# Performance work log

Hardware: AMD Instinct MI355X
Metric: run time of the kernel (lower is better)

Reference implementation:

```python
import jax, jax.numpy as jnp
import numpy as np

N = 50000      # nodes
E = 600000     # edges
D_IN = 128
D_H = 128
D_OUT = 64
HEADS = 2
NEG_SLOPE = 0.2  # PyG GATConv default leaky_relu slope
BN_EPS = 1e-5


def setup_inputs() -> dict:
    key = jax.random.key(0)
    ks = jax.random.split(key, 24)
    w = lambda i, shape: (jax.random.normal(ks[i], shape, jnp.float32) * 0.1)
    return {
        "x": jax.random.normal(ks[0], (N, D_IN), jnp.float32),
        "edge_index": jax.random.randint(ks[1], (2, E), 0, N, jnp.int64),
        "W_gcn1": w(2, (D_IN, D_H)),
        "b_gcn1": jnp.zeros((D_H,), jnp.float32),
        "bn1_gamma": jax.random.uniform(ks[3], (D_H,), jnp.float32, 0.5, 1.5),
        "bn1_beta": w(4, (D_H,)),
        "bn1_mean": w(5, (D_H,)),
        "bn1_var": jax.random.uniform(ks[6], (D_H,), jnp.float32, 0.5, 1.5),
        "W_gat1": w(7, (D_H, HEADS * D_H)),
        "a_src1": w(8, (HEADS, D_H)),
        "a_dst1": w(9, (HEADS, D_H)),
        "b_gat1": jnp.zeros((D_H,), jnp.float32),
        "W_gcn2": w(10, (D_H, D_H)),
        "b_gcn2": jnp.zeros((D_H,), jnp.float32),
        "bn2_gamma": jax.random.uniform(ks[11], (D_H,), jnp.float32, 0.5, 1.5),
        "bn2_beta": w(12, (D_H,)),
        "bn2_mean": w(13, (D_H,)),
        "bn2_var": jax.random.uniform(ks[14], (D_H,), jnp.float32, 0.5, 1.5),
        "W_gat2": w(15, (D_H, HEADS * D_OUT)),
        "a_src2": w(16, (HEADS, D_OUT)),
        "a_dst2": w(17, (HEADS, D_OUT)),
        "b_gat2": jnp.zeros((D_OUT,), jnp.float32),
    }


def _add_self_loops(edge_index):
    loop = jnp.arange(N, dtype=edge_index.dtype)
    src = jnp.concatenate([edge_index[0], loop])
    dst = jnp.concatenate([edge_index[1], loop])
    return src, dst


def _gcn(x, edge_index, W, b):
    # PyG GCNConv: add self-loops, symmetric D^-1/2 (A+I) D^-1/2 normalization
    src, dst = _add_self_loops(edge_index)
    deg = jax.ops.segment_sum(jnp.ones_like(dst, x.dtype), dst, num_segments=N)
    dinv = jax.lax.rsqrt(jnp.maximum(deg, 1.0))  # deg >= 1 with self-loops
    norm = dinv[src] * dinv[dst]                 # [E+N]
    h = x @ W                                    # [N, C]
    out = jax.ops.segment_sum(h[src] * norm[:, None], dst, num_segments=N)
    return out + b


def _gat(x, edge_index, W, a_src, a_dst, b, out_ch):
    # PyG GATConv (concat=False): per-head attention, segment softmax over dst,
    # mean across heads. Dropout off (eval mode).
    h = (x @ W).reshape(N, HEADS, out_ch)                 # [N, H, C]
    al_s = jnp.einsum('nhc,hc->nh', h, a_src)             # [N, H]
    al_d = jnp.einsum('nhc,hc->nh', h, a_dst)             # [N, H]
    src, dst = _add_self_loops(edge_index)
    e = al_s[src] + al_d[dst]                             # [E+N, H]
    e = jnp.where(e > 0, e, NEG_SLOPE * e)                # leaky_relu
    m = jax.ops.segment_max(e, dst, num_segments=N)       # [N, H]
    ex = jnp.exp(e - m[dst])
    denom = jax.ops.segment_sum(ex, dst, num_segments=N)  # [N, H]
    alpha = ex / denom[dst]                               # [E+N, H]
    out = jax.ops.segment_sum(h[src] * alpha[:, :, None], dst, num_segments=N)
    return out.mean(axis=1) + b                           # concat=False -> mean


def _bn_eval(x, gamma, beta, mean, var):
    return (x - mean) * jax.lax.rsqrt(var + BN_EPS) * gamma + beta


def reference(x, edge_index, W_gcn1, b_gcn1, bn1_gamma, bn1_beta, bn1_mean, bn1_var,
              W_gat1, a_src1, a_dst1, b_gat1, W_gcn2, b_gcn2,
              bn2_gamma, bn2_beta, bn2_mean, bn2_var,
              W_gat2, a_src2, a_dst2, b_gat2):
    h = _gcn(x, edge_index, W_gcn1, b_gcn1)
    h = jax.nn.relu(_bn_eval(h, bn1_gamma, bn1_beta, bn1_mean, bn1_var))
    h = jax.nn.relu(_gat(h, edge_index, W_gat1, a_src1, a_dst1, b_gat1, D_H))
    h = _gcn(h, edge_index, W_gcn2, b_gcn2)
    h = jax.nn.relu(_bn_eval(h, bn2_gamma, bn2_beta, bn2_mean, bn2_var))
    h = _gat(h, edge_index, W_gat2, a_src2, a_dst2, b_gat2, D_OUT)
    return jax.nn.log_softmax(h, axis=1)
```

## Files before the change

kernel.cpp:

```cpp
#include <hip/hip_runtime.h>
#include <hip/hip_bf16.h>

#define N_NODES 50000
#define N_EDGES 600000

typedef short bf16x8 __attribute__((ext_vector_type(8)));
typedef float f32x4 __attribute__((ext_vector_type(4)));

__device__ __forceinline__ float leaky(float e) { return fmaxf(e, 0.2f * e); }
__device__ __forceinline__ unsigned short f2b(float f) {
  __hip_bfloat16 h = __float2bfloat16(f);
  return *reinterpret_cast<unsigned short*>(&h);
}
__device__ __forceinline__ float blo(unsigned int u) { return __uint_as_float(u << 16); }
__device__ __forceinline__ float bhi(unsigned int u) { return __uint_as_float(u & 0xffff0000u); }

__global__ void k_convert(const int* __restrict__ e, int* __restrict__ src32,
                          int* __restrict__ dst32, int* __restrict__ deg,
                          const float* __restrict__ W1, const float* __restrict__ WG1,
                          const float* __restrict__ W2, const float* __restrict__ WG2,
                          unsigned short* __restrict__ Wt1, unsigned short* __restrict__ WtG1,
                          unsigned short* __restrict__ Wt2, unsigned short* __restrict__ WtG2,
                          const float* b1, const float* g1, const float* be1, const float* m1,
                          const float* v1, const float* b2, const float* g2, const float* be2,
                          const float* m2, const float* v2, float* sc1, float* sh1,
                          float* sc2, float* sh2,
                          const float* as1, const float* ad1, const float* as2,
                          const float* ad2, float* was1, float* wad1, float* was2,
                          float* wad2) {
  __shared__ int sflag;
  int tid = threadIdx.x;
  if (tid < 64) {
    int idx = 1 + 2 * tid * 4096;
    int v = e[idx];
    unsigned long long nz = __ballot(v != 0);
    if (tid == 0) sflag = (nz == 0ULL) ? 1 : 0;
  }
  __syncthreads();
  int f = sflag;
  int i = blockIdx.x * 256 + tid;
  if (i < N_EDGES) {
    int s, d;
    if (f) { s = e[2 * i]; d = e[2 * (N_EDGES + i)]; }
    else   { s = e[i];     d = e[N_EDGES + i]; }
    src32[i] = s;
    dst32[i] = d;
    atomicAdd(&deg[d], 1);
  }
  if (i < 16384) {
    int k = i >> 7, c = i & 127;
    Wt1[c * 128 + k] = f2b(W1[i]);
  } else if (i < 49152) {
    int l = i - 16384;
    int k = l >> 8, c = l & 255;
    WtG1[c * 128 + k] = f2b(WG1[l]);
  } else if (i < 65536) {
    int l = i - 49152;
    int k = l >> 7, c = l & 127;
    Wt2[c * 128 + k] = f2b(W2[l]);
  } else if (i < 81920) {
    int l = i - 65536;
    int k = l >> 7, c = l & 127;
    WtG2[c * 128 + k] = f2b(WG2[l]);
  } else if (i < 82048) {
    int c = i - 81920;
    float s = g1[c] * rsqrtf(v1[c] + 1e-5f);
    sc1[c] = s;
    sh1[c] = (b1[c] - m1[c]) * s + be1[c];
  } else if (i < 82176) {
    int c = i - 82048;
    float s = g2[c] * rsqrtf(v2[c] + 1e-5f);
    sc2[c] = s;
    sh2[c] = (b2[c] - m2[c]) * s + be2[c];
  } else if (i < 82688) {
    int j = i - 82176;
    int k = j & 127;
    int vec = j >> 7;
    const float* Wr = (vec < 2) ? (WG1 + k * 256) : (WG2 + k * 128);
    const float* av = (vec == 0) ? as1 : (vec == 1) ? ad1 : (vec == 2) ? as2 : ad2;
    float* op = (vec == 0) ? was1 : (vec == 1) ? wad1 : (vec == 2) ? was2 : wad2;
    int hl = (vec < 2) ? 128 : 64;
    float s0 = 0.f, s1 = 0.f;
    for (int c = 0; c < hl; c += 4) {
      float4 wv = *(const float4*)(Wr + c);
      float4 a4 = *(const float4*)(av + c);
      s0 += wv.x * a4.x + wv.y * a4.y + wv.z * a4.z + wv.w * a4.w;
    }
    for (int c = 0; c < hl; c += 4) {
      float4 wv = *(const float4*)(Wr + hl + c);
      float4 a4 = *(const float4*)(av + hl + c);
      s1 += wv.x * a4.x + wv.y * a4.y + wv.z * a4.z + wv.w * a4.w;
    }
    op[2 * k] = s0;
    op[2 * k + 1] = s1;
  }
}

__global__ void k_offsets(const int* __restrict__ deg, int* __restrict__ gbase,
                          int* __restrict__ roff, int* __restrict__ cursor,
                          float* __restrict__ dinv) {
  __shared__ int s[256];
  __shared__ int base;
  int t = threadIdx.x;
  int i = blockIdx.x * 256 + t;
  int v = (i < N_NODES) ? deg[i] : 0;
  s[t] = v;
  __syncthreads();
  for (int o = 1; o < 256; o <<= 1) {
    int x = (t >= o) ? s[t - o] : 0;
    __syncthreads();
    s[t] += x;
    __syncthreads();
  }
  if (t == 255) base = atomicAdd(gbase, s[255]);
  __syncthreads();
  int off = base + s[t] - v;
  if (i < N_NODES) {
    roff[i] = off;
    cursor[i] = off;
    dinv[i] = rsqrtf((float)v + 1.f);
  }
}
__global__ void k_fill(const int* __restrict__ src, const int* __restrict__ dst,
                       int* __restrict__ cursor, int2* __restrict__ aen,
                       const float* __restrict__ dinv) {
  int e = blockIdx.x * 256 + threadIdx.x;
  if (e < N_EDGES) {
    int s = src[e], d = dst[e];
    int pos = atomicAdd(&cursor[d], 1);
    aen[pos] = make_int2(s, __float_as_int(dinv[s]));
  }
}

__device__ __forceinline__ float4 ld4(const float* X, size_t idx) {
  return *(const float4*)(X + idx);
}
__device__ __forceinline__ float4 ld4(const unsigned short* X, size_t idx) {
  uint2 r = *(const uint2*)(X + idx);
  return make_float4(blo(r.x), bhi(r.x), blo(r.y), bhi(r.y));
}

template <int C, typename TX>
__global__ __launch_bounds__(256, 4) void gemm_mfma(const TX* __restrict__ X,
                                                    const unsigned short* __restrict__ Wt,
                                                    unsigned short* __restrict__ Hb) {
  constexpr int CTW = C / 64;
  __shared__ __align__(16) short smem[64 * 136];
  int tid = threadIdx.x;
  int row0 = blockIdx.x * 64;
  for (int i = tid; i < 2048; i += 256) {
    int r = i >> 5;
    int k4 = (i & 31) * 4;
    int row = row0 + r;
    float4 v = make_float4(0.f, 0.f, 0.f, 0.f);
    if (row < N_NODES) v = ld4(X, (size_t)row * 128 + k4);
    uint2 p;
    p.x = (unsigned int)f2b(v.x) | ((unsigned int)f2b(v.y) << 16);
    p.y = (unsigned int)f2b(v.z) | ((unsigned int)f2b(v.w) << 16);
    *(uint2*)&smem[r * 136 + k4] = p;
  }
  int wave = tid >> 6, lane = tid & 63;
  int m = lane & 15, quad = lane >> 4;
  int c0 = wave * (16 * CTW);
  bf16x8 b[CTW][4];
#pragma unroll
  for (int ct = 0; ct < CTW; ++ct) {
    const unsigned short* wp = Wt + (size_t)(c0 + ct * 16 + m) * 128 + quad * 8;
#pragma unroll
    for (int kk = 0; kk < 4; ++kk) b[ct][kk] = *(const bf16x8*)(wp + kk * 32);
  }
  __syncthreads();
#pragma unroll
  for (int rt = 0; rt < 4; ++rt) {
    bf16x8 a[4];
#pragma unroll
    for (int kk = 0; kk < 4; ++kk)
      a[kk] = *(const bf16x8*)&smem[(rt * 16 + m) * 136 + kk * 32 + quad * 8];
    f32x4 acc[CTW];
#pragma unroll
    for (int ct = 0; ct < CTW; ++ct) acc[ct] = (f32x4){0.f, 0.f, 0.f, 0.f};
#pragma unroll
    for (int ct = 0; ct < CTW; ++ct)
#pragma unroll
      for (int kk = 0; kk < 4; ++kk)
        acc[ct] = __builtin_amdgcn_mfma_f32_16x16x32_bf16(a[kk], b[ct][kk], acc[ct], 0, 0, 0);
    int rbase = row0 + rt * 16 + quad * 4;
#pragma unroll
    for (int ct = 0; ct < CTW; ++ct) {
#pragma unroll
      for (int reg = 0; reg < 4; ++reg) {
        int row = rbase + reg;
        if (row < N_NODES)
          Hb[(size_t)row * C + c0 + ct * 16 + m] = f2b(acc[ct][reg]);
      }
    }
  }
}

__global__ __launch_bounds__(256) void gcn_pull(const unsigned short* __restrict__ Hb,
                                                const int2* __restrict__ aen,
                                                const int* __restrict__ roff,
                                                const int* __restrict__ deg,
                                                const float* __restrict__ dinv,
                                                const float* __restrict__ sc,
                                                const float* __restrict__ sh,
                                                const float* __restrict__ was,
                                                const float* __restrict__ wad,
                                                float* __restrict__ als,
                                                float* __restrict__ ald,
                                                unsigned short* __restrict__ out) {
  int wv = (blockIdx.x * 256 + threadIdx.x) >> 6;
  int lane = threadIdx.x & 63;
  int q4 = lane >> 4, l16 = lane & 15;
  int qb = lane & 48, l7 = lane & 7;
  int i = 4 * wv + q4;
  if (i >= N_NODES) return;
  int off = roff[i], end = off + deg[i];
  float di = dinv[i];
  uint4 u = *(const uint4*)((const char*)Hb + (unsigned)i * 256u + l16 * 16u);
  float a0 = blo(u.x) * di, a1 = bhi(u.x) * di;
  float a2 = blo(u.y) * di, a3 = bhi(u.y) * di;
  float a4 = blo(u.z) * di, a5 = bhi(u.z) * di;
  float a6 = blo(u.w) * di, a7 = bhi(u.w) * di;
  int j = off;
  int nfull = (end - off) >> 3;
  int2 ae = make_int2(i, 0);
  if (l7 < end - j) ae = aen[j + l7];
  for (int t = 0; t < nfull; ++t) {
    int ss[8];
#pragma unroll
    for (int k = 0; k < 8; ++k) ss[k] = __shfl(ae.x, qb + k, 64);
    float ww[8];
#pragma unroll
    for (int k = 0; k < 8; ++k) ww[k] = __shfl(__int_as_float(ae.y), qb + k, 64);
    uint4 vv[8];
#pragma unroll
    for (int k = 0; k < 8; ++k)
      vv[k] = *(const uint4*)((const char*)Hb + (unsigned)ss[k] * 256u + l16 * 16u);
    j += 8;
    if (l7 < end - j) ae = aen[j + l7];
#pragma unroll
    for (int k = 0; k < 8; ++k) {
      a0 = fmaf(blo(vv[k].x), ww[k], a0); a1 = fmaf(bhi(vv[k].x), ww[k], a1);
      a2 = fmaf(blo(vv[k].y), ww[k], a2); a3 = fmaf(bhi(vv[k].y), ww[k], a3);
      a4 = fmaf(blo(vv[k].z), ww[k], a4); a5 = fmaf(bhi(vv[k].z), ww[k], a5);
      a6 = fmaf(blo(vv[k].w), ww[k], a6); a7 = fmaf(bhi(vv[k].w), ww[k], a7);
    }
  }
  int rem = end - j;
  if (rem) {
    int ss[8];
#pragma unroll
    for (int k = 0; k < 8; ++k) ss[k] = __shfl(ae.x, qb + k, 64);
    float ww[8];
#pragma unroll
    for (int k = 0; k < 8; ++k) ww[k] = __shfl(__int_as_float(ae.y), qb + k, 64);
    uint4 vv[8];
#pragma unroll
    for (int k = 0; k < 8; ++k)
      if (k < rem)
        vv[k] = *(const uint4*)((const char*)Hb + (unsigned)ss[k] * 256u + l16 * 16u);
#pragma unroll
    for (int k = 0; k < 8; ++k)
      if (k < rem) {
        a0 = fmaf(blo(vv[k].x), ww[k], a0); a1 = fmaf(bhi(vv[k].x), ww[k], a1);
        a2 = fmaf(blo(vv[k].y), ww[k], a2); a3 = fmaf(bhi(vv[k].y), ww[k], a3);
        a4 = fmaf(blo(vv[k].z), ww[k], a4); a5 = fmaf(bhi(vv[k].z), ww[k], a5);
        a6 = fmaf(blo(vv[k].w), ww[k], a6); a7 = fmaf(bhi(vv[k].w), ww[k], a7);
      }
  }
  int c0 = l16 * 8;
  float4 sca = *(const float4*)(sc + c0), scb = *(const float4*)(sc + c0 + 4);
  float4 sha = *(const float4*)(sh + c0), shb = *(const float4*)(sh + c0 + 4);
  float t0 = fmaxf(fmaf(a0 * di, sca.x, sha.x), 0.f);
  float t1 = fmaxf(fmaf(a1 * di, sca.y, sha.y), 0.f);
  float t2 = fmaxf(fmaf(a2 * di, sca.z, sha.z), 0.f);
  float t3 = fmaxf(fmaf(a3 * di, sca.w, sha.w), 0.f);
  float t4 = fmaxf(fmaf(a4 * di, scb.x, shb.x), 0.f);
  float t5 = fmaxf(fmaf(a5 * di, scb.y, shb.y), 0.f);
  float t6 = fmaxf(fmaf(a6 * di, scb.z, shb.z), 0.f);
  float t7 = fmaxf(fmaf(a7 * di, scb.w, shb.w), 0.f);
  float4 w0 = *(const float4*)(was + 2 * c0);
  float4 w1 = *(const float4*)(was + 2 * c0 + 4);
  float4 w2 = *(const float4*)(was + 2 * c0 + 8);
  float4 w3 = *(const float4*)(was + 2 * c0 + 12);
  float sl0 = t0 * w0.x + t1 * w0.z + t2 * w1.x + t3 * w1.z +
              t4 * w2.x + t5 * w2.z + t6 * w3.x + t7 * w3.z;
  float sl1 = t0 * w0.y + t1 * w0.w + t2 * w1.y + t3 * w1.w +
              t4 * w2.y + t5 * w2.w + t6 * w3.y + t7 * w3.w;
  w0 = *(const float4*)(wad + 2 * c0);
  w1 = *(const float4*)(wad + 2 * c0 + 4);
  w2 = *(const float4*)(wad + 2 * c0 + 8);
  w3 = *(const float4*)(wad + 2 * c0 + 12);
  float dl0 = t0 * w0.x + t1 * w0.z + t2 * w1.x + t3 * w1.z +
              t4 * w2.x + t5 * w2.z + t6 * w3.x + t7 * w3.z;
  float dl1 = t0 * w0.y + t1 * w0.w + t2 * w1.y + t3 * w1.w +
              t4 * w2.y + t5 * w2.w + t6 * w3.y + t7 * w3.w;
#pragma unroll
  for (int mask = 1; mask <= 8; mask <<= 1) {
    sl0 += __shfl_xor(sl0, mask, 64);
    sl1 += __shfl_xor(sl1, mask, 64);
    dl0 += __shfl_xor(dl0, mask, 64);
    dl1 += __shfl_xor(dl1, mask, 64);
  }
  if (l16 == 0) {
    *(float2*)(als + 2 * i) = make_float2(sl0, sl1);
    *(float2*)(ald + 2 * i) = make_float2(dl0, dl1);
  }
  uint4 pw;
  pw.x = (unsigned int)f2b(t0) | ((unsigned int)f2b(t1) << 16);
  pw.y = (unsigned int)f2b(t2) | ((unsigned int)f2b(t3) << 16);
  pw.z = (unsigned int)f2b(t4) | ((unsigned int)f2b(t5) << 16);
  pw.w = (unsigned int)f2b(t6) | ((unsigned int)f2b(t7) << 16);
  *(uint4*)(out + (size_t)i * 128 + l16 * 8) = pw;
}

__global__ __launch_bounds__(256) void gat_pull128(const unsigned short* __restrict__ Hb,
                                                   const int2* __restrict__ aen,
                                                   const int* __restrict__ roff,
                                                   const int* __restrict__ deg,
                                                   const float* __restrict__ als,
                                                   const float* __restrict__ ald,
                                                   const float* __restrict__ bias,
                                                   unsigned short* __restrict__ out) {
  int wv = (blockIdx.x * 256 + threadIdx.x) >> 6;
  int lane = threadIdx.x & 63;
  int half = lane >> 5, l = lane & 31;
  int hbase = lane & 32, l7 = lane & 7;
  int i = 2 * wv + half;
  if (i >= N_NODES) return;
  int off = roff[i], end = off + deg[i];
  int head = l >> 4;
  float2 dif = *(const float2*)(ald + 2 * i);
  float p = 0.f;
  float acc0 = 0.f, acc1 = 0.f, acc2 = 0.f, acc3 = 0.f;
  float acc4 = 0.f, acc5 = 0.f, acc6 = 0.f, acc7 = 0.f;
  int j = off;
  int nfull = (end - off) >> 3;
  int2 ae = make_int2(i, 0);
  float2 av = make_float2(-1e30f, -1e30f);
  if (l7 < end - j) {
    ae = aen[j + l7];
    av = *(const float2*)(als + 2 * ae.x);
  }
  for (int t = 0; t < nfull; ++t) {
    int ss[8];
#pragma unroll
    for (int k = 0; k < 8; ++k) ss[k] = __shfl(ae.x, hbase + k, 64);
    uint4 vv[8];
#pragma unroll
    for (int k = 0; k < 8; ++k)
      vv[k] = *(const uint4*)((const char*)Hb + (unsigned)ss[k] * 512u + l * 16u);
    float q0 = __expf(leaky(av.x + dif.x));
    float q1 = __expf(leaky(av.y + dif.y));
    j += 8;
    if (l7 < end - j) {
      ae = aen[j + l7];
      av = *(const float2*)(als + 2 * ae.x);
    }
#pragma unroll
    for (int k = 0; k < 8; ++k) {
      float b0 = __shfl(q0, hbase + k, 64);
      float b1 = __shfl(q1, hbase + k, 64);
      float q = head ? b1 : b0;
      p += q;
      acc0 = fmaf(q, blo(vv[k].x), acc0); acc1 = fmaf(q, bhi(vv[k].x), acc1);
      acc2 = fmaf(q, blo(vv[k].y), acc2); acc3 = fmaf(q, bhi(vv[k].y), acc3);
      acc4 = fmaf(q, blo(vv[k].z), acc4); acc5 = fmaf(q, bhi(vv[k].z), acc5);
      acc6 = fmaf(q, blo(vv[k].w), acc6); acc7 = fmaf(q, bhi(vv[k].w), acc7);
    }
  }
  int rem = end - j;
  if (rem) {
    int ss[8];
#pragma unroll
    for (int k = 0; k < 8; ++k) ss[k] = __shfl(ae.x, hbase + k, 64);
    uint4 vv[8];
#pragma unroll
    for (int k = 0; k < 8; ++k)
      if (k < rem)
        vv[k] = *(const uint4*)((const char*)Hb + (unsigned)ss[k] * 512u + l * 16u);
    float q0 = __expf(leaky(av.x + dif.x));
    float q1 = __expf(leaky(av.y + dif.y));
#pragma unroll
    for (int k = 0; k < 8; ++k)
      if (k < rem) {
        float b0 = __shfl(q0, hbase + k, 64);
        float b1 = __shfl(q1, hbase + k, 64);
        float q = head ? b1 : b0;
        p += q;
        acc0 = fmaf(q, blo(vv[k].x), acc0); acc1 = fmaf(q, bhi(vv[k].x), acc1);
        acc2 = fmaf(q, blo(vv[k].y), acc2); acc3 = fmaf(q, bhi(vv[k].y), acc3);
        acc4 = fmaf(q, blo(vv[k].z), acc4); acc5 = fmaf(q, bhi(vv[k].z), acc5);
        acc6 = fmaf(q, blo(vv[k].w), acc6); acc7 = fmaf(q, bhi(vv[k].w), acc7);
      }
  }
  float2 ai = *(const float2*)(als + 2 * i);
  float axs = head ? ai.y : ai.x;
  float dh = head ? dif.y : dif.x;
  float es = __expf(leaky(axs + dh));
  float rsel = 0.5f / (p + es);
  uint4 u = *(const uint4*)((const char*)Hb + (unsigned)i * 512u + l * 16u);
  acc0 = (acc0 + es * blo(u.x)) * rsel; acc1 = (acc1 + es * bhi(u.x)) * rsel;
  acc2 = (acc2 + es * blo(u.y)) * rsel; acc3 = (acc3 + es * bhi(u.y)) * rsel;
  acc4 = (acc4 + es * blo(u.z)) * rsel; acc5 = (acc5 + es * bhi(u.z)) * rsel;
  acc6 = (acc6 + es * blo(u.w)) * rsel; acc7 = (acc7 + es * bhi(u.w)) * rsel;
  acc0 += __shfl_xor(acc0, 16, 64); acc1 += __shfl_xor(acc1, 16, 64);
  acc2 += __shfl_xor(acc2, 16, 64); acc3 += __shfl_xor(acc3, 16, 64);
  acc4 += __shfl_xor(acc4, 16, 64); acc5 += __shfl_xor(acc5, 16, 64);
  acc6 += __shfl_xor(acc6, 16, 64); acc7 += __shfl_xor(acc7, 16, 64);
  if (head == 0) {
    int c = l * 8;
    float4 b0 = *(const float4*)(bias + c);
    float4 b1 = *(const float4*)(bias + c + 4);
    uint4 pw;
    pw.x = (unsigned int)f2b(fmaxf(acc0 + b0.x, 0.f)) |
           ((unsigned int)f2b(fmaxf(acc1 + b0.y, 0.f)) << 16);
    pw.y = (unsigned int)f2b(fmaxf(acc2 + b0.z, 0.f)) |
           ((unsigned int)f2b(fmaxf(acc3 + b0.w, 0.f)) << 16);
    pw.z = (unsigned int)f2b(fmaxf(acc4 + b1.x, 0.f)) |
           ((unsigned int)f2b(fmaxf(acc5 + b1.y, 0.f)) << 16);
    pw.w = (unsigned int)f2b(fmaxf(acc6 + b1.z, 0.f)) |
           ((unsigned int)f2b(fmaxf(acc7 + b1.w, 0.f)) << 16);
    *(uint4*)(out + (size_t)i * 128 + c) = pw;
  }
}

__global__ __launch_bounds__(256) void gat_pull64_lsm(const unsigned short* __restrict__ Hb,
                                                      const int2* __restrict__ aen,
                                                      const int* __restrict__ roff,
                                                      const int* __restrict__ deg,
                                                      const float* __restrict__ als,
                                                      const float* __restrict__ ald,
                                                      const float* __restrict__ bias,
                                                      float* __restrict__ out) {
  int wv = (blockIdx.x * 256 + threadIdx.x) >> 6;
  int lane = threadIdx.x & 63;
  int q4 = lane >> 4, l16 = lane & 15;
  int qb = lane & 48, l7 = lane & 7;
  int hh = l16 >> 3, p8 = l16 & 7;
  int i = 4 * wv + q4;
  if (i >= N_NODES) return;
  int off = roff[i], end = off + deg[i];
  unsigned cb2 = (unsigned)(hh * 64 + 8 * p8) * 2u;
  float2 dd = *(const float2*)(ald + 2 * i);
  float p = 0.f;
  float acc0 = 0.f, acc1 = 0.f, acc2 = 0.f, acc3 = 0.f;
  float acc4 = 0.f, acc5 = 0.f, acc6 = 0.f, acc7 = 0.f;
  int j = off;
  int nfull = (end - off) >> 3;
  int2 ae = make_int2(i, 0);
  float2 av = make_float2(-1e30f, -1e30f);
  if (l7 < end - j) {
    ae = aen[j + l7];
    av = *(const float2*)(als + 2 * ae.x);
  }
  for (int t = 0; t < nfull; ++t) {
    int ss[8];
#pragma unroll
    for (int k = 0; k < 8; ++k) ss[k] = __shfl(ae.x, qb + k, 64);
    uint4 vv[8];
#pragma unroll
    for (int k = 0; k < 8; ++k)
      vv[k] = *(const uint4*)((const char*)Hb + (unsigned)ss[k] * 256u + cb2);
    float q0 = __expf(leaky(av.x + dd.x));
    float q1 = __expf(leaky(av.y + dd.y));
    j += 8;
    if (l7 < end - j) {
      ae = aen[j + l7];
      av = *(const float2*)(als + 2 * ae.x);
    }
#pragma unroll
    for (int k = 0; k < 8; ++k) {
      float b0 = __shfl(q0, qb + k, 64);
      float b1 = __shfl(q1, qb + k, 64);
      float q = hh ? b1 : b0;
      p += q;
      acc0 = fmaf(q, blo(vv[k].x), acc0); acc1 = fmaf(q, bhi(vv[k].x), acc1);
      acc2 = fmaf(q, blo(vv[k].y), acc2); acc3 = fmaf(q, bhi(vv[k].y), acc3);
      acc4 = fmaf(q, blo(vv[k].z), acc4); acc5 = fmaf(q, bhi(vv[k].z), acc5);
      acc6 = fmaf(q, blo(vv[k].w), acc6); acc7 = fmaf(q, bhi(vv[k].w), acc7);
    }
  }
  int rem = end - j;
  if (rem) {
    int ss[8];
#pragma unroll
    for (int k = 0; k < 8; ++k) ss[k] = __shfl(ae.x, qb + k, 64);
    uint4 vv[8];
#pragma unroll
    for (int k = 0; k < 8; ++k)
      if (k < rem)
        vv[k] = *(const uint4*)((const char*)Hb + (unsigned)ss[k] * 256u + cb2);
    float q0 = __expf(leaky(av.x + dd.x));
    float q1 = __expf(leaky(av.y + dd.y));
#pragma unroll
    for (int k = 0; k < 8; ++k)
      if (k < rem) {
        float b0 = __shfl(q0, qb + k, 64);
        float b1 = __shfl(q1, qb + k, 64);
        float q = hh ? b1 : b0;
        p += q;
        acc0 = fmaf(q, blo(vv[k].x), acc0); acc1 = fmaf(q, bhi(vv[k].x), acc1);
        acc2 = fmaf(q, blo(vv[k].y), acc2); acc3 = fmaf(q, bhi(vv[k].y), acc3);
        acc4 = fmaf(q, blo(vv[k].z), acc4); acc5 = fmaf(q, bhi(vv[k].z), acc5);
        acc6 = fmaf(q, blo(vv[k].w), acc6); acc7 = fmaf(q, bhi(vv[k].w), acc7);
      }
  }
  float2 ai = *(const float2*)(als + 2 * i);
  float axs = hh ? ai.y : ai.x;
  float dh = hh ? dd.y : dd.x;
  float es = __expf(leaky(axs + dh));
  float rsel = 0.5f / (p + es);
  uint4 u = *(const uint4*)((const char*)Hb + (unsigned)i * 256u + cb2);
  acc0 = (acc0 + es * blo(u.x)) * rsel; acc1 = (acc1 + es * bhi(u.x)) * rsel;
  acc2 = (acc2 + es * blo(u.y)) * rsel; acc3 = (acc3 + es * bhi(u.y)) * rsel;
  acc4 = (acc4 + es * blo(u.z)) * rsel; acc5 = (acc5 + es * bhi(u.z)) * rsel;
  acc6 = (acc6 + es * blo(u.w)) * rsel; acc7 = (acc7 + es * bhi(u.w)) * rsel;
  acc0 += __shfl_xor(acc0, 8, 64); acc1 += __shfl_xor(acc1, 8, 64);
  acc2 += __shfl_xor(acc2, 8, 64); acc3 += __shfl_xor(acc3, 8, 64);
  acc4 += __shfl_xor(acc4, 8, 64); acc5 += __shfl_xor(acc5, 8, 64);
  acc6 += __shfl_xor(acc6, 8, 64); acc7 += __shfl_xor(acc7, 8, 64);
  float4 b0 = *(const float4*)(bias + 8 * p8);
  float4 b1 = *(const float4*)(bias + 8 * p8 + 4);
  float v0 = acc0 + b0.x, v1 = acc1 + b0.y, v2 = acc2 + b0.z, v3 = acc3 + b0.w;
  float v4 = acc4 + b1.x, v5 = acc5 + b1.y, v6 = acc6 + b1.z, v7 = acc7 + b1.w;
  float mv = fmaxf(fmaxf(fmaxf(v0, v1), fmaxf(v2, v3)),
                   fmaxf(fmaxf(v4, v5), fmaxf(v6, v7)));
#pragma unroll
  for (int mm = 4; mm > 0; mm >>= 1) mv = fmaxf(mv, __shfl_xor(mv, mm, 64));
  float sv = __expf(v0 - mv) + __expf(v1 - mv) + __expf(v2 - mv) + __expf(v3 - mv) +
             __expf(v4 - mv) + __expf(v5 - mv) + __expf(v6 - mv) + __expf(v7 - mv);
#pragma unroll
  for (int mm = 4; mm > 0; mm >>= 1) sv += __shfl_xor(sv, mm, 64);
  float ls = mv + __logf(sv);
  if (hh == 0) {
    *(float4*)(out + (size_t)i * 64 + 8 * p8) =
        make_float4(v0 - ls, v1 - ls, v2 - ls, v3 - ls);
    *(float4*)(out + (size_t)i * 64 + 8 * p8 + 4) =
        make_float4(v4 - ls, v5 - ls, v6 - ls, v7 - ls);
  }
}

extern "C" void kernel_launch(void* const* d_in, const int* in_sizes, int n_in, void* d_out,
                              int out_size, void* d_ws, size_t ws_size, hipStream_t stream) {
  const float* x      = (const float*)d_in[0];
  const int* eidx     = (const int*)d_in[1];
  const float* W_gcn1 = (const float*)d_in[2];
  const float* b_gcn1 = (const float*)d_in[3];
  const float* bn1_g  = (const float*)d_in[4];
  const float* bn1_b  = (const float*)d_in[5];
  const float* bn1_m  = (const float*)d_in[6];
  const float* bn1_v  = (const float*)d_in[7];
  const float* W_gat1 = (const float*)d_in[8];
  const float* a_src1 = (const float*)d_in[9];
  const float* a_dst1 = (const float*)d_in[10];
  const float* b_gat1 = (const float*)d_in[11];
  const float* W_gcn2 = (const float*)d_in[12];
  const float* b_gcn2 = (const float*)d_in[13];
  const float* bn2_g  = (const float*)d_in[14];
  const float* bn2_b  = (const float*)d_in[15];
  const float* bn2_m  = (const float*)d_in[16];
  const float* bn2_v  = (const float*)d_in[17];
  const float* W_gat2 = (const float*)d_in[18];
  const float* a_src2 = (const float*)d_in[19];
  const float* a_dst2 = (const float*)d_in[20];
  const float* b_gat2 = (const float*)d_in[21];

  char* ws = (char*)d_ws;
  size_t o = 0;
  auto take = [&](size_t bytes) {
    char* p = ws + o;
    o = (o + bytes + 255) & ~(size_t)255;
    return p;
  };
  int* srcs    = (int*)take((size_t)N_EDGES * 4);
  int* dstsb   = (int*)take((size_t)N_EDGES * 4);
  int* deg     = (int*)take((size_t)(N_NODES + 64) * 4);
  int* gbase   = deg + N_NODES;
  int* roff    = (int*)take((size_t)N_NODES * 4);
  int* cursor  = (int*)take((size_t)N_NODES * 4);
  int2* aen    = (int2*)take((size_t)N_EDGES * 8);
  float* dinv  = (float*)take((size_t)N_NODES * 4);
  float* als   = (float*)take((size_t)2 * N_NODES * 4);
  float* ald   = (float*)take((size_t)2 * N_NODES * 4);
  float* sc1   = (float*)take(128 * 4);
  float* sh1   = (float*)take(128 * 4);
  float* sc2   = (float*)take(128 * 4);
  float* sh2   = (float*)take(128 * 4);
  float* was1  = (float*)take(256 * 4);
  float* wad1  = (float*)take(256 * 4);
  float* was2  = (float*)take(256 * 4);
  float* wad2  = (float*)take(256 * 4);
  unsigned short* Wt1  = (unsigned short*)take((size_t)128 * 128 * 2);
  unsigned short* WtG1 = (unsigned short*)take((size_t)256 * 128 * 2);
  unsigned short* Wt2  = (unsigned short*)take((size_t)128 * 128 * 2);
  unsigned short* WtG2 = (unsigned short*)take((size_t)128 * 128 * 2);
  unsigned short* Hb   = (unsigned short*)take((size_t)N_NODES * 256 * 2);
  unsigned short* Pb   = (unsigned short*)take((size_t)N_NODES * 128 * 2);
  (void)ws_size; (void)in_sizes; (void)n_in; (void)out_size;

  int eb = (N_EDGES + 255) / 256;
  int nb = (N_NODES + 255) / 256;
  int hb = ((N_NODES + 1) / 2 + 3) / 4;
  int qb = ((N_NODES + 3) / 4 + 3) / 4;
  int gb = (N_NODES + 63) / 64;

  hipMemsetAsync(deg, 0, (size_t)(N_NODES + 1) * 4, stream);
  k_convert<<<eb, 256, 0, stream>>>(eidx, srcs, dstsb, deg, W_gcn1, W_gat1, W_gcn2, W_gat2,
                                    Wt1, WtG1, Wt2, WtG2, b_gcn1, bn1_g, bn1_b, bn1_m, bn1_v,
                                    b_gcn2, bn2_g, bn2_b, bn2_m, bn2_v, sc1, sh1, sc2, sh2,
                                    a_src1, a_dst1, a_src2, a_dst2, was1, wad1, was2, wad2);
  k_offsets<<<nb, 256, 0, stream>>>(deg, gbase, roff, cursor, dinv);
  k_fill<<<eb, 256, 0, stream>>>(srcs, dstsb, cursor, aen, dinv);

  gemm_mfma<128><<<gb, 256, 0, stream>>>(x, Wt1, Hb);
  gcn_pull<<<qb, 256, 0, stream>>>(Hb, aen, roff, deg, dinv, sc1, sh1, was1, wad1,
                                   als, ald, Pb);
  gemm_mfma<256><<<gb, 256, 0, stream>>>(Pb, WtG1, Hb);
  gat_pull128<<<hb, 256, 0, stream>>>(Hb, aen, roff, deg, als, ald, b_gat1, Pb);
  gemm_mfma<128><<<gb, 256, 0, stream>>>(Pb, Wt2, Hb);
  gcn_pull<<<qb, 256, 0, stream>>>(Hb, aen, roff, deg, dinv, sc2, sh2, was2, wad2,
                                   als, ald, Pb);
  gemm_mfma<128><<<gb, 256, 0, stream>>>(Pb, WtG2, Hb);
  gat_pull64_lsm<<<qb, 256, 0, stream>>>(Hb, aen, roff, deg, als, ald, b_gat2,
                                         (float*)d_out);
}
```

Baseline: 364.8 us.

## Reorder GAT1 to aggregate 128-wide inputs before the head projection

Result: faster. 340.8 us (-6.6%).

```diff
diff --git a/kernel.cpp b/kernel.cpp
--- a/kernel.cpp
+++ b/kernel.cpp
@@ -52,8 +52,9 @@
     Wt1[c * 128 + k] = f2b(W1[i]);
   } else if (i < 49152) {
     int l = i - 16384;
-    int k = l >> 8, c = l & 255;
-    WtG1[c * 128 + k] = f2b(WG1[l]);
+    int k = l >> 8, c8 = l & 255;
+    int head = c8 >> 7, cc = c8 & 127;
+    WtG1[cc * 256 + head * 128 + k] = f2b(WG1[l]);
   } else if (i < 65536) {
     int l = i - 49152;
     int k = l >> 7, c = l & 127;
@@ -140,11 +141,10 @@
   return make_float4(blo(r.x), bhi(r.x), blo(r.y), bhi(r.y));
 }
 
-template <int C, typename TX>
+template <typename TX>
 __global__ __launch_bounds__(256, 4) void gemm_mfma(const TX* __restrict__ X,
                                                     const unsigned short* __restrict__ Wt,
                                                     unsigned short* __restrict__ Hb) {
-  constexpr int CTW = C / 64;
   __shared__ __align__(16) short smem[64 * 136];
   int tid = threadIdx.x;
   int row0 = blockIdx.x * 64;
@@ -161,10 +161,10 @@
   }
   int wave = tid >> 6, lane = tid & 63;
   int m = lane & 15, quad = lane >> 4;
-  int c0 = wave * (16 * CTW);
-  bf16x8 b[CTW][4];
-#pragma unroll
-  for (int ct = 0; ct < CTW; ++ct) {
+  int c0 = wave * 32;
+  bf16x8 b[2][4];
+#pragma unroll
+  for (int ct = 0; ct < 2; ++ct) {
     const unsigned short* wp = Wt + (size_t)(c0 + ct * 16 + m) * 128 + quad * 8;
 #pragma unroll
     for (int kk = 0; kk < 4; ++kk) b[ct][kk] = *(const bf16x8*)(wp + kk * 32);
@@ -176,22 +176,88 @@
 #pragma unroll
     for (int kk = 0; kk < 4; ++kk)
       a[kk] = *(const bf16x8*)&smem[(rt * 16 + m) * 136 + kk * 32 + quad * 8];
-    f32x4 acc[CTW];
-#pragma unroll
-    for (int ct = 0; ct < CTW; ++ct) acc[ct] = (f32x4){0.f, 0.f, 0.f, 0.f};
-#pragma unroll
-    for (int ct = 0; ct < CTW; ++ct)
+    f32x4 acc[2];
+#pragma unroll
+    for (int ct = 0; ct < 2; ++ct) acc[ct] = (f32x4){0.f, 0.f, 0.f, 0.f};
+#pragma unroll
+    for (int ct = 0; ct < 2; ++ct)
 #pragma unroll
       for (int kk = 0; kk < 4; ++kk)
         acc[ct] = __builtin_amdgcn_mfma_f32_16x16x32_bf16(a[kk], b[ct][kk], acc[ct], 0, 0, 0);
     int rbase = row0 + rt * 16 + quad * 4;
 #pragma unroll
-    for (int ct = 0; ct < CTW; ++ct) {
+    for (int ct = 0; ct < 2; ++ct) {
 #pragma unroll
       for (int reg = 0; reg < 4; ++reg) {
         int row = rbase + reg;
         if (row < N_NODES)
-          Hb[(size_t)row * C + c0 + ct * 16 + m] = f2b(acc[ct][reg]);
+          Hb[(size_t)row * 128 + c0 + ct * 16 + m] = f2b(acc[ct][reg]);
+      }
+    }
+  }
+}
+
+__global__ __launch_bounds__(256, 4) void gemm_k256(const unsigned short* __restrict__ Q,
+                                                    const unsigned short* __restrict__ Wt,
+                                                    const float* __restrict__ bias,
+                                                    unsigned short* __restrict__ G) {
+  __shared__ __align__(16) short smem[64 * 136];
+  int tid = threadIdx.x;
+  int row0 = blockIdx.x * 64;
+  int wave = tid >> 6, lane = tid & 63;
+  int m = lane & 15, quad = lane >> 4;
+  int c0 = wave * 32;
+  f32x4 acc[4][2];
+#pragma unroll
+  for (int rt = 0; rt < 4; ++rt)
+#pragma unroll
+    for (int ct = 0; ct < 2; ++ct) acc[rt][ct] = (f32x4){0.f, 0.f, 0.f, 0.f};
+#pragma unroll
+  for (int half = 0; half < 2; ++half) {
+    if (half) __syncthreads();
+    for (int i = tid; i < 2048; i += 256) {
+      int r = i >> 5;
+      int k4 = (i & 31) * 4;
+      int row = row0 + r;
+      uint2 p = make_uint2(0u, 0u);
+      if (row < N_NODES) p = *(const uint2*)(Q + (size_t)row * 256 + half * 128 + k4);
+      *(uint2*)&smem[r * 136 + k4] = p;
+    }
+    bf16x8 b[2][4];
+#pragma unroll
+    for (int ct = 0; ct < 2; ++ct) {
+      const unsigned short* wp =
+          Wt + (size_t)(c0 + ct * 16 + m) * 256 + half * 128 + quad * 8;
+#pragma unroll
+      for (int kk = 0; kk < 4; ++kk) b[ct][kk] = *(const bf16x8*)(wp + kk * 32);
+    }
+    __syncthreads();
+#pragma unroll
+    for (int rt = 0; rt < 4; ++rt) {
+      bf16x8 a[4];
+#pragma unroll
+      for (int kk = 0; kk < 4; ++kk)
+        a[kk] = *(const bf16x8*)&smem[(rt * 16 + m) * 136 + kk * 32 + quad * 8];
+#pragma unroll
+      for (int ct = 0; ct < 2; ++ct)
+#pragma unroll
+        for (int kk = 0; kk < 4; ++kk)
+          acc[rt][ct] =
+              __builtin_amdgcn_mfma_f32_16x16x32_bf16(a[kk], b[ct][kk], acc[rt][ct], 0, 0, 0);
+    }
+  }
+#pragma unroll
+  for (int rt = 0; rt < 4; ++rt) {
+    int rbase = row0 + rt * 16 + quad * 4;
+#pragma unroll
+    for (int ct = 0; ct < 2; ++ct) {
+      int col = c0 + ct * 16 + m;
+      float bs = bias[col];
+#pragma unroll
+      for (int reg = 0; reg < 4; ++reg) {
+        int row = rbase + reg;
+        if (row < N_NODES)
+          G[(size_t)row * 128 + col] = f2b(fmaxf(acc[rt][ct][reg] + bs, 0.f));
       }
     }
   }
@@ -315,26 +381,26 @@
   *(uint4*)(out + (size_t)i * 128 + l16 * 8) = pw;
 }
 
-__global__ __launch_bounds__(256) void gat_pull128(const unsigned short* __restrict__ Hb,
-                                                   const int2* __restrict__ aen,
-                                                   const int* __restrict__ roff,
-                                                   const int* __restrict__ deg,
-                                                   const float* __restrict__ als,
-                                                   const float* __restrict__ ald,
-                                                   const float* __restrict__ bias,
-                                                   unsigned short* __restrict__ out) {
+__global__ __launch_bounds__(256) void gat1_pull(const unsigned short* __restrict__ P,
+                                                 const int2* __restrict__ aen,
+                                                 const int* __restrict__ roff,
+                                                 const int* __restrict__ deg,
+                                                 const float* __restrict__ als,
+                                                 const float* __restrict__ ald,
+                                                 unsigned short* __restrict__ Q) {
   int wv = (blockIdx.x * 256 + threadIdx.x) >> 6;
   int lane = threadIdx.x & 63;
-  int half = lane >> 5, l = lane & 31;
-  int hbase = lane & 32, l7 = lane & 7;
-  int i = 2 * wv + half;
+  int q4 = lane >> 4, l16 = lane & 15;
+  int qb = lane & 48, l7 = lane & 7;
+  int i = 4 * wv + q4;
   if (i >= N_NODES) return;
   int off = roff[i], end = off + deg[i];
-  int head = l >> 4;
   float2 dif = *(const float2*)(ald + 2 * i);
-  float p = 0.f;
-  float acc0 = 0.f, acc1 = 0.f, acc2 = 0.f, acc3 = 0.f;
-  float acc4 = 0.f, acc5 = 0.f, acc6 = 0.f, acc7 = 0.f;
+  float p0 = 0.f, p1 = 0.f;
+  float g0 = 0.f, g1 = 0.f, g2 = 0.f, g3 = 0.f,
+        g4 = 0.f, g5 = 0.f, g6 = 0.f, g7 = 0.f;
+  float h0 = 0.f, h1 = 0.f, h2 = 0.f, h3 = 0.f,
+        h4 = 0.f, h5 = 0.f, h6 = 0.f, h7 = 0.f;
   int j = off;
   int nfull = (end - off) >> 3;
   int2 ae = make_int2(i, 0);
@@ -346,11 +412,11 @@
   for (int t = 0; t < nfull; ++t) {
     int ss[8];
 #pragma unroll
-    for (int k = 0; k < 8; ++k) ss[k] = __shfl(ae.x, hbase + k, 64);
+    for (int k = 0; k < 8; ++k) ss[k] = __shfl(ae.x, qb + k, 64);
     uint4 vv[8];
 #pragma unroll
     for (int k = 0; k < 8; ++k)
-      vv[k] = *(const uint4*)((const char*)Hb + (unsigned)ss[k] * 512u + l * 16u);
+      vv[k] = *(const uint4*)((const char*)P + (unsigned)ss[k] * 256u + l16 * 16u);
     float q0 = __expf(leaky(av.x + dif.x));
     float q1 = __expf(leaky(av.y + dif.y));
     j += 8;
@@ -360,70 +426,82 @@
     }
 #pragma unroll
     for (int k = 0; k < 8; ++k) {
-      float b0 = __shfl(q0, hbase + k, 64);
-      float b1 = __shfl(q1, hbase + k, 64);
-      float q = head ? b1 : b0;
-      p += q;
-      acc0 = fmaf(q, blo(vv[k].x), acc0); acc1 = fmaf(q, bhi(vv[k].x), acc1);
-      acc2 = fmaf(q, blo(vv[k].y), acc2); acc3 = fmaf(q, bhi(vv[k].y), acc3);
-      acc4 = fmaf(q, blo(vv[k].z), acc4); acc5 = fmaf(q, bhi(vv[k].z), acc5);
-      acc6 = fmaf(q, blo(vv[k].w), acc6); acc7 = fmaf(q, bhi(vv[k].w), acc7);
+      float b0 = __shfl(q0, qb + k, 64);
+      float b1 = __shfl(q1, qb + k, 64);
+      p0 += b0; p1 += b1;
+      float c0 = blo(vv[k].x), c1 = bhi(vv[k].x);
+      float c2 = blo(vv[k].y), c3 = bhi(vv[k].y);
+      float c4 = blo(vv[k].z), c5 = bhi(vv[k].z);
+      float c6 = blo(vv[k].w), c7 = bhi(vv[k].w);
+      g0 = fmaf(b0, c0, g0); h0 = fmaf(b1, c0, h0);
+      g1 = fmaf(b0, c1, g1); h1 = fmaf(b1, c1, h1);
+      g2 = fmaf(b0, c2, g2); h2 = fmaf(b1, c2, h2);
+      g3 = fmaf(b0, c3, g3); h3 = fmaf(b1, c3, h3);
+      g4 = fmaf(b0, c4, g4); h4 = fmaf(b1, c4, h4);
+      g5 = fmaf(b0, c5, g5); h5 = fmaf(b1, c5, h5);
+      g6 = fmaf(b0, c6, g6); h6 = fmaf(b1, c6, h6);
+      g7 = fmaf(b0, c7, g7); h7 = fmaf(b1, c7, h7);
     }
   }
   int rem = end - j;
   if (rem) {
     int ss[8];
 #pragma unroll
-    for (int k = 0; k < 8; ++k) ss[k] = __shfl(ae.x, hbase + k, 64);
+    for (int k = 0; k < 8; ++k) ss[k] = __shfl(ae.x, qb + k, 64);
     uint4 vv[8];
 #pragma unroll
     for (int k = 0; k < 8; ++k)
       if (k < rem)
-        vv[k] = *(const uint4*)((const char*)Hb + (unsigned)ss[k] * 512u + l * 16u);
+        vv[k] = *(const uint4*)((const char*)P + (unsigned)ss[k] * 256u + l16 * 16u);
     float q0 = __expf(leaky(av.x + dif.x));
     float q1 = __expf(leaky(av.y + dif.y));
 #pragma unroll
     for (int k = 0; k < 8; ++k)
       if (k < rem) {
-        float b0 = __shfl(q0, hbase + k, 64);
-        float b1 = __shfl(q1, hbase + k, 64);
-        float q = head ? b1 : b0;
-        p += q;
-        acc0 = fmaf(q, blo(vv[k].x), acc0); acc1 = fmaf(q, bhi(vv[k].x), acc1);
-        acc2 = fmaf(q, blo(vv[k].y), acc2); acc3 = fmaf(q, bhi(vv[k].y), acc3);
-        acc4 = fmaf(q, blo(vv[k].z), acc4); acc5 = fmaf(q, bhi(vv[k].z), acc5);
-        acc6 = fmaf(q, blo(vv[k].w), acc6); acc7 = fmaf(q, bhi(vv[k].w), acc7);
+        float b0 = __shfl(q0, qb + k, 64);
+        float b1 = __shfl(q1, qb + k, 64);
+        p0 += b0; p1 += b1;
+        float c0 = blo(vv[k].x), c1 = bhi(vv[k].x);
+        float c2 = blo(vv[k].y), c3 = bhi(vv[k].y);
+        float c4 = blo(vv[k].z), c5 = bhi(vv[k].z);
+        float c6 = blo(vv[k].w), c7 = bhi(vv[k].w);
+        g0 = fmaf(b0, c0, g0); h0 = fmaf(b1, c0, h0);
+        g1 = fmaf(b0, c1, g1); h1 = fmaf(b1, c1, h1);
+        g2 = fmaf(b0, c2, g2); h2 = fmaf(b1, c2, h2);
+        g3 = fmaf(b0, c3, g3); h3 = fmaf(b1, c3, h3);
+        g4 = fmaf(b0, c4, g4); h4 = fmaf(b1, c4, h4);
+        g5 = fmaf(b0, c5, g5); h5 = fmaf(b1, c5, h5);
+        g6 = fmaf(b0, c6, g6); h6 = fmaf(b1, c6, h6);
+        g7 = fmaf(b0, c7, g7); h7 = fmaf(b1, c7, h7);
       }
   }
   float2 ai = *(const float2*)(als + 2 * i);
-  float axs = head ? ai.y : ai.x;
-  float dh = head ? dif.y : dif.x;
-  float es = __expf(leaky(axs + dh));
-  float rsel = 0.5f / (p + es);
-  uint4 u = *(const uint4*)((const char*)Hb + (unsigned)i * 512u + l * 16u);
-  acc0 = (acc0 + es * blo(u.x)) * rsel; acc1 = (acc1 + es * bhi(u.x)) * rsel;
-  acc2 = (acc2 + es * blo(u.y)) * rsel; acc3 = (acc3 + es * bhi(u.y)) * rsel;
-  acc4 = (acc4 + es * blo(u.z)) * rsel; acc5 = (acc5 + es * bhi(u.z)) * rsel;
-  acc6 = (acc6 + es * blo(u.w)) * rsel; acc7 = (acc7 + es * bhi(u.w)) * rsel;
-  acc0 += __shfl_xor(acc0, 16, 64); acc1 += __shfl_xor(acc1, 16, 64);
-  acc2 += __shfl_xor(acc2, 16, 64); acc3 += __shfl_xor(acc3, 16, 64);
-  acc4 += __shfl_xor(acc4, 16, 64); acc5 += __shfl_xor(acc5, 16, 64);
-  acc6 += __shfl_xor(acc6, 16, 64); acc7 += __shfl_xor(acc7, 16, 64);
-  if (head == 0) {
-    int c = l * 8;
-    float4 b0 = *(const float4*)(bias + c);
-    float4 b1 = *(const float4*)(bias + c + 4);
-    uint4 pw;
-    pw.x = (unsigned int)f2b(fmaxf(acc0 + b0.x, 0.f)) |
-           ((unsigned int)f2b(fmaxf(acc1 + b0.y, 0.f)) << 16);
-    pw.y = (unsigned int)f2b(fmaxf(acc2 + b0.z, 0.f)) |
-           ((unsigned int)f2b(fmaxf(acc3 + b0.w, 0.f)) << 16);
-    pw.z = (unsigned int)f2b(fmaxf(acc4 + b1.x, 0.f)) |
-           ((unsigned int)f2b(fmaxf(acc5 + b1.y, 0.f)) << 16);
-    pw.w = (unsigned int)f2b(fmaxf(acc6 + b1.z, 0.f)) |
-           ((unsigned int)f2b(fmaxf(acc7 + b1.w, 0.f)) << 16);
-    *(uint4*)(out + (size_t)i * 128 + c) = pw;
-  }
+  float es0 = __expf(leaky(ai.x + dif.x));
+  float es1 = __expf(leaky(ai.y + dif.y));
+  float r0 = 0.5f / (p0 + es0);
+  float r1 = 0.5f / (p1 + es1);
+  uint4 u = *(const uint4*)((const char*)P + (unsigned)i * 256u + l16 * 16u);
+  float c0 = blo(u.x), c1 = bhi(u.x), c2 = blo(u.y), c3 = bhi(u.y);
+  float c4 = blo(u.z), c5 = bhi(u.z), c6 = blo(u.w), c7 = bhi(u.w);
+  g0 = (g0 + es0 * c0) * r0; g1 = (g1 + es0 * c1) * r0;
+  g2 = (g2 + es0 * c2) * r0; g3 = (g3 + es0 * c3) * r0;
+  g4 = (g4 + es0 * c4) * r0; g5 = (g5 + es0 * c5) * r0;
+  g6 = (g6 + es0 * c6) * r0; g7 = (g7 + es0 * c7) * r0;
+  h0 = (h0 + es1 * c0) * r1; h1 = (h1 + es1 * c1) * r1;
+  h2 = (h2 + es1 * c2) * r1; h3 = (h3 + es1 * c3) * r1;
+  h4 = (h4 + es1 * c4) * r1; h5 = (h5 + es1 * c5) * r1;
+  h6 = (h6 + es1 * c6) * r1; h7 = (h7 + es1 * c7) * r1;
+  uint4 pw;
+  pw.x = (unsigned int)f2b(g0) | ((unsigned int)f2b(g1) << 16);
+  pw.y = (unsigned int)f2b(g2) | ((unsigned int)f2b(g3) << 16);
+  pw.z = (unsigned int)f2b(g4) | ((unsigned int)f2b(g5) << 16);
+  pw.w = (unsigned int)f2b(g6) | ((unsigned int)f2b(g7) << 16);
+  *(uint4*)(Q + (size_t)i * 256 + l16 * 8) = pw;
+  pw.x = (unsigned int)f2b(h0) | ((unsigned int)f2b(h1) << 16);
+  pw.y = (unsigned int)f2b(h2) | ((unsigned int)f2b(h3) << 16);
+  pw.z = (unsigned int)f2b(h4) | ((unsigned int)f2b(h5) << 16);
+  pw.w = (unsigned int)f2b(h6) | ((unsigned int)f2b(h7) << 16);
+  *(uint4*)(Q + (size_t)i * 256 + 128 + l16 * 8) = pw;
 }
 
 __global__ __launch_bounds__(256) void gat_pull64_lsm(const unsigned short* __restrict__ Hb,
@@ -593,16 +671,17 @@
   float* was2  = (float*)take(256 * 4);
   float* wad2  = (float*)take(256 * 4);
   unsigned short* Wt1  = (unsigned short*)take((size_t)128 * 128 * 2);
-  unsigned short* WtG1 = (unsigned short*)take((size_t)256 * 128 * 2);
+  unsigned short* WtG1 = (unsigned short*)take((size_t)128 * 256 * 2);
   unsigned short* Wt2  = (unsigned short*)take((size_t)128 * 128 * 2);
   unsigned short* WtG2 = (unsigned short*)take((size_t)128 * 128 * 2);
-  unsigned short* Hb   = (unsigned short*)take((size_t)N_NODES * 256 * 2);
+  unsigned short* Hb   = (unsigned short*)take((size_t)N_NODES * 128 * 2);
   unsigned short* Pb   = (unsigned short*)take((size_t)N_NODES * 128 * 2);
+  unsigned short* Qb   = (unsigned short*)take((size_t)N_NODES * 256 * 2);
+  unsigned short* Gb   = (unsigned short*)take((size_t)N_NODES * 128 * 2);
   (void)ws_size; (void)in_sizes; (void)n_in; (void)out_size;
 
   int eb = (N_EDGES + 255) / 256;
   int nb = (N_NODES + 255) / 256;
-  int hb = ((N_NODES + 1) / 2 + 3) / 4;
   int qb = ((N_NODES + 3) / 4 + 3) / 4;
   int gb = (N_NODES + 63) / 64;
 
@@ -614,15 +693,15 @@
   k_offsets<<<nb, 256, 0, stream>>>(deg, gbase, roff, cursor, dinv);
   k_fill<<<eb, 256, 0, stream>>>(srcs, dstsb, cursor, aen, dinv);
 
-  gemm_mfma<128><<<gb, 256, 0, stream>>>(x, Wt1, Hb);
+  gemm_mfma<<<gb, 256, 0, stream>>>(x, Wt1, Hb);
   gcn_pull<<<qb, 256, 0, stream>>>(Hb, aen, roff, deg, dinv, sc1, sh1, was1, wad1,
                                    als, ald, Pb);
-  gemm_mfma<256><<<gb, 256, 0, stream>>>(Pb, WtG1, Hb);
-  gat_pull128<<<hb, 256, 0, stream>>>(Hb, aen, roff, deg, als, ald, b_gat1, Pb);
-  gemm_mfma<128><<<gb, 256, 0, stream>>>(Pb, Wt2, Hb);
+  gat1_pull<<<qb, 256, 0, stream>>>(Pb, aen, roff, deg, als, ald, Qb);
+  gemm_k256<<<gb, 256, 0, stream>>>(Qb, WtG1, b_gat1, Gb);
+  gemm_mfma<<<gb, 256, 0, stream>>>(Gb, Wt2, Hb);
   gcn_pull<<<qb, 256, 0, stream>>>(Hb, aen, roff, deg, dinv, sc2, sh2, was2, wad2,
                                    als, ald, Pb);
-  gemm_mfma<128><<<gb, 256, 0, stream>>>(Pb, WtG2, Hb);
-  gat_pull64_lsm<<<qb, 256, 0, stream>>>(Hb, aen, roff, deg, als, ald, b_gat2,
+  gemm_mfma<<<gb, 256, 0, stream>>>(Pb, WtG2, Qb);
+  gat_pull64_lsm<<<qb, 256, 0, stream>>>(Qb, aen, roff, deg, als, ald, b_gat2,
                                          (float*)d_out);
 }
```
